# Kernel optimization log

Hardware: AMD Instinct MI355X
Metric: run time of the kernel (lower is better)

## Reference

```python
import jax, jax.numpy as jnp
import numpy as np

BATCH, LENGTH, IN, STATE, OUT = 8, 4096, 512, 256, 512


def setup_inputs() -> dict:
    key = jax.random.key(0)
    k1, k2, k3, k4, k5 = jax.random.split(key, 5)
    u = jax.random.normal(k1, (BATCH, LENGTH, IN), dtype=jnp.float32)
    x0 = jax.random.normal(k2, (BATCH, STATE), dtype=jnp.float32)
    A = 0.9999 * (2.0 * jax.random.uniform(k3, (STATE,), dtype=jnp.float32) - 1.0)
    B = jax.random.normal(k4, (IN, STATE), dtype=jnp.float32) / (STATE + IN) ** 0.5
    C = jax.random.normal(k5, (STATE, OUT), dtype=jnp.float32) / STATE ** 0.5
    return {"u": u, "x0": x0, "A": A, "B": B, "C": C}


def reference(u, x0, A, B, C):
    L = u.shape[1]
    # A_powers[t, n] = A[n] ** t, shape [L, state]
    A_powers = jnp.power(A[None, :], jnp.arange(L, dtype=u.dtype)[:, None])
    uB = u @ B  # [batch, L, state]
    # FFT convolution; inputs are real so rfft/irfft gives same result as
    # real(ifft(fft*fft)) in the original.
    T = 2 ** int(np.ceil(np.log2(2 * L - 1)))
    Af = jnp.fft.rfft(A_powers, n=T, axis=0)  # [T/2+1, state]
    Uf = jnp.fft.rfft(uB, n=T, axis=1)        # [batch, T/2+1, state]
    x = jnp.fft.irfft(Af[None, :, :] * Uf, n=T, axis=1)[:, :L]  # [batch, L, state]
    # initial-state contribution: A * A_powers * x0
    x = x + A[None, None, :] * A_powers[None, :, :] * x0[:, None, :]
    y = x @ C  # [batch, L, out]
    return (y, x[:, -1])
```

## Files before the change

kernel.cpp:

```cpp
#include <hip/hip_runtime.h>

#define BATCH   8
#define LENGTH  4096
#define IN_DIM  512
#define STATE   256
#define OUT_DIM 512
#define NC      64
#define LC      64

typedef __attribute__((ext_vector_type(8)))  short bf16x8;
typedef __attribute__((ext_vector_type(16))) float f32x16;

union FragU { bf16x8 v; unsigned u[4]; };

__device__ __forceinline__ unsigned short bf16_rne(float v) {
    unsigned u = __builtin_bit_cast(unsigned, v);
    unsigned r = (u + 0x7FFFu + ((u >> 16) & 1u)) >> 16;
    return (unsigned short)r;
}
__device__ __forceinline__ float bf16_f(unsigned short h) {
    unsigned u = ((unsigned)h) << 16;
    return __builtin_bit_cast(float, u);
}

__global__ __launch_bounds__(256) void split_T_kernel(
    const float* __restrict__ in, unsigned short* __restrict__ hi,
    unsigned short* __restrict__ lo, int kbits, int Nsrc)
{
    int id = blockIdx.x * 256 + threadIdx.x;
    int k = id & ((1 << kbits) - 1);
    int n = id >> kbits;
    float v = in[(size_t)k * Nsrc + n];
    unsigned short h = bf16_rne(v);
    hi[id] = h;
    lo[id] = bf16_rne(v - bf16_f(h));
}

__global__ __launch_bounds__(256, 2) void gemm_dbuf(
    const float* __restrict__ Af, const unsigned short* __restrict__ Bthi,
    const unsigned short* __restrict__ Btlo, float* __restrict__ Cc,
    int N_, int K)
{
    __shared__ unsigned short lds[2 * 16384];

    const int tid  = threadIdx.x;
    const int wave = tid >> 6;
    const int lane = tid & 63;
    const int n0 = blockIdx.x * 128;
    const int m0 = blockIdx.y * 128;

    const char* gp[8];
    int ldsoff[8], gstep[8];
    #pragma unroll
    for (int t = 0; t < 8; ++t) {
        int gi = wave * 8 + t;
        if (gi < 16) {
            int p = gi * 64 + lane;
            int row = p >> 3, s = p & 7;
            int l = s ^ (row & 7);
            gp[t] = (const char*)(Af + (size_t)(m0 + row) * K + l * 4);
            gstep[t] = 32 * 4;
            ldsoff[t] = gi * 512;
        } else {
            int q2 = (gi - 16) >> 3;
            int pi = (gi - 16) & 7;
            int p = pi * 64 + lane;
            int row = p >> 2, s = p & 3;
            int l = s ^ ((row >> 1) & 3);
            const unsigned short* base = q2 ? Btlo : Bthi;
            gp[t] = (const char*)(base + (size_t)(n0 + row) * K + l * 8);
            gstep[t] = 32 * 2;
            ldsoff[t] = 8192 + q2 * 4096 + pi * 512;
        }
    }

    const int l31 = lane & 31, q2 = lane >> 5;
    const int wm = (wave >> 1) * 64, wn = (wave & 1) * 64;

    int aoff[2][2][2];
    #pragma unroll
    for (int mi = 0; mi < 2; ++mi) {
        int row = wm + mi * 32 + l31;
        #pragma unroll
        for (int ks = 0; ks < 2; ++ks)
            #pragma unroll
            for (int h = 0; h < 2; ++h)
                aoff[mi][ks][h] = row * 64 + ((ks * 4 + q2 * 2 + h) ^ (row & 7)) * 8;
    }
    int boff[2][2];
    #pragma unroll
    for (int nj = 0; nj < 2; ++nj) {
        int row = wn + nj * 32 + l31;
        #pragma unroll
        for (int ks = 0; ks < 2; ++ks)
            boff[nj][ks] = row * 32 + (((ks * 2 + q2) ^ ((row >> 1) & 3))) * 8;
    }

    f32x16 acc[2][2];
    #pragma unroll
    for (int mi = 0; mi < 2; ++mi)
        #pragma unroll
        for (int nj = 0; nj < 2; ++nj)
            #pragma unroll
            for (int r = 0; r < 16; ++r) acc[mi][nj][r] = 0.f;

    #pragma unroll
    for (int t = 0; t < 8; ++t) {
        __builtin_amdgcn_global_load_lds(
            (const __attribute__((address_space(1))) unsigned*)(gp[t]),
            (__attribute__((address_space(3))) unsigned*)(&lds[ldsoff[t]]),
            16, 0, 0);
        gp[t] += gstep[t];
    }

    const int nit = K >> 5;
    for (int it = 0; it < nit; ++it) {
        asm volatile("" ::: "memory");
        __builtin_amdgcn_s_barrier();
        asm volatile("" ::: "memory");
        if (it + 1 < nit) {
            const int bb = ((it + 1) & 1) * 16384;
            #pragma unroll
            for (int t = 0; t < 8; ++t) {
                __builtin_amdgcn_global_load_lds(
                    (const __attribute__((address_space(1))) unsigned*)(gp[t]),
                    (__attribute__((address_space(3))) unsigned*)(&lds[bb + ldsoff[t]]),
                    16, 0, 0);
                gp[t] += gstep[t];
            }
            __builtin_amdgcn_s_waitcnt(0x0F78);
        } else {
            __builtin_amdgcn_s_waitcnt(0x0F70);
        }
        asm volatile("" ::: "memory");
        __builtin_amdgcn_s_barrier();
        asm volatile("" ::: "memory");

        const unsigned short* buf = &lds[(it & 1) * 16384];

        #pragma unroll
        for (int ks = 0; ks < 2; ++ks) {
            FragU ahi[2], alo[2];
            #pragma unroll
            for (int mi = 0; mi < 2; ++mi) {
                float4 f0 = *(const float4*)(buf + aoff[mi][ks][0]);
                float4 f1 = *(const float4*)(buf + aoff[mi][ks][1]);
                unsigned b0 = __builtin_bit_cast(unsigned, f0.x);
                unsigned b1 = __builtin_bit_cast(unsigned, f0.y);
                unsigned b2 = __builtin_bit_cast(unsigned, f0.z);
                unsigned b3 = __builtin_bit_cast(unsigned, f0.w);
                unsigned b4 = __builtin_bit_cast(unsigned, f1.x);
                unsigned b5 = __builtin_bit_cast(unsigned, f1.y);
                unsigned b6 = __builtin_bit_cast(unsigned, f1.z);
                unsigned b7 = __builtin_bit_cast(unsigned, f1.w);
                ahi[mi].u[0] = __builtin_amdgcn_perm(b1, b0, 0x07060302);
                ahi[mi].u[1] = __builtin_amdgcn_perm(b3, b2, 0x07060302);
                ahi[mi].u[2] = __builtin_amdgcn_perm(b5, b4, 0x07060302);
                ahi[mi].u[3] = __builtin_amdgcn_perm(b7, b6, 0x07060302);
                float l0 = f0.x - __builtin_bit_cast(float, b0 & 0xFFFF0000u);
                float l1 = f0.y - __builtin_bit_cast(float, b1 & 0xFFFF0000u);
                float l2 = f0.z - __builtin_bit_cast(float, b2 & 0xFFFF0000u);
                float l3 = f0.w - __builtin_bit_cast(float, b3 & 0xFFFF0000u);
                float l4 = f1.x - __builtin_bit_cast(float, b4 & 0xFFFF0000u);
                float l5 = f1.y - __builtin_bit_cast(float, b5 & 0xFFFF0000u);
                float l6 = f1.z - __builtin_bit_cast(float, b6 & 0xFFFF0000u);
                float l7 = f1.w - __builtin_bit_cast(float, b7 & 0xFFFF0000u);
                alo[mi].u[0] = __builtin_amdgcn_perm(
                    __builtin_bit_cast(unsigned, l1), __builtin_bit_cast(unsigned, l0), 0x07060302);
                alo[mi].u[1] = __builtin_amdgcn_perm(
                    __builtin_bit_cast(unsigned, l3), __builtin_bit_cast(unsigned, l2), 0x07060302);
                alo[mi].u[2] = __builtin_amdgcn_perm(
                    __builtin_bit_cast(unsigned, l5), __builtin_bit_cast(unsigned, l4), 0x07060302);
                alo[mi].u[3] = __builtin_amdgcn_perm(
                    __builtin_bit_cast(unsigned, l7), __builtin_bit_cast(unsigned, l6), 0x07060302);
            }
            FragU bhi[2], blo[2];
            #pragma unroll
            for (int nj = 0; nj < 2; ++nj) {
                bhi[nj].v = *(const bf16x8*)(buf +  8192 + boff[nj][ks]);
                blo[nj].v = *(const bf16x8*)(buf + 12288 + boff[nj][ks]);
            }
            #pragma unroll
            for (int mi = 0; mi < 2; ++mi)
                #pragma unroll
                for (int nj = 0; nj < 2; ++nj) {
                    acc[mi][nj] = __builtin_amdgcn_mfma_f32_32x32x16_bf16(
                        ahi[mi].v, bhi[nj].v, acc[mi][nj], 0, 0, 0);
                    acc[mi][nj] = __builtin_amdgcn_mfma_f32_32x32x16_bf16(
                        alo[mi].v, bhi[nj].v, acc[mi][nj], 0, 0, 0);
                    acc[mi][nj] = __builtin_amdgcn_mfma_f32_32x32x16_bf16(
                        ahi[mi].v, blo[nj].v, acc[mi][nj], 0, 0, 0);
                }
        }
    }

    #pragma unroll
    for (int mi = 0; mi < 2; ++mi)
        #pragma unroll
        for (int nj = 0; nj < 2; ++nj) {
            #pragma unroll
            for (int r = 0; r < 16; ++r) {
                int row_g = m0 + wm + mi * 32 + 4 * q2 + (r & 3) + 8 * (r >> 2);
                int col_g = n0 + wn + nj * 32 + l31;
                Cc[(size_t)row_g * N_ + col_g] = acc[mi][nj][r];
            }
        }
}

__global__ __launch_bounds__(256) void scan_carry(
    const float* __restrict__ uB, const float* __restrict__ A,
    float* __restrict__ carry)
{
    const int b = blockIdx.x;
    const int c = blockIdx.y;
    const int n = threadIdx.x;
    const float a = A[n];
    const float* p = uB + ((size_t)b * LENGTH + (size_t)c * LC) * STATE + n;
    float s = 0.f;
    #pragma unroll 8
    for (int j = 0; j < LC; ++j) s = a * s + p[(size_t)j * STATE];
    carry[((size_t)b * NC + c) * STATE + n] = s;
}

__global__ __launch_bounds__(256) void scan_apply(
    const float* __restrict__ uB, const float* __restrict__ A,
    const float* __restrict__ carry, const float* __restrict__ x0,
    float* __restrict__ x, float* __restrict__ x_last)
{
    const int b = blockIdx.x;
    const int c = blockIdx.y;
    const int n = threadIdx.x;
    const float a = A[n];
    float a2 = a * a, a4 = a2 * a2, a8 = a4 * a4, a16 = a8 * a8, a32 = a16 * a16;
    const float aLC = a32 * a32;

    float s = x0[(size_t)b * STATE + n];
    for (int d = 0; d < c; ++d)
        s = aLC * s + carry[((size_t)b * NC + d) * STATE + n];

    const size_t base = ((size_t)b * LENGTH + (size_t)c * LC) * STATE + n;
    const float* p = uB + base;
    float* qx = x + base;
    #pragma unroll 8
    for (int j = 0; j < LC; ++j) {
        s = a * s + p[(size_t)j * STATE];
        qx[(size_t)j * STATE] = s;
    }
    if (c == NC - 1) x_last[(size_t)b * STATE + n] = s;
}

extern "C" void kernel_launch(void* const* d_in, const int* in_sizes, int n_in,
                              void* d_out, int out_size, void* d_ws, size_t ws_size,
                              hipStream_t stream)
{
    const float* u  = (const float*)d_in[0];
    const float* x0 = (const float*)d_in[1];
    const float* A  = (const float*)d_in[2];
    const float* B  = (const float*)d_in[3];
    const float* C  = (const float*)d_in[4];

    const size_t MB = 1024 * 1024;
    char* ws = (char*)d_ws;

    float* x     = (float*)(ws);
    float* carry = (float*)(ws + 32 * MB);
    unsigned short* Bt_hi = (unsigned short*)(ws + 33 * MB);
    unsigned short* Bt_lo = (unsigned short*)(ws + 33 * MB + 256 * 1024);
    unsigned short* Ct_hi = (unsigned short*)(ws + 33 * MB + 512 * 1024);
    unsigned short* Ct_lo = (unsigned short*)(ws + 33 * MB + 768 * 1024);

    float* y      = (float*)d_out;
    float* x_last = y + (size_t)BATCH * LENGTH * OUT_DIM;
    float* uB     = (float*)((char*)d_out + 32 * MB);

    const int M = BATCH * LENGTH;

    split_T_kernel<<<dim3((IN_DIM * STATE) / 256), dim3(256), 0, stream>>>(B, Bt_hi, Bt_lo, 9, STATE);
    split_T_kernel<<<dim3((STATE * OUT_DIM) / 256), dim3(256), 0, stream>>>(C, Ct_hi, Ct_lo, 8, OUT_DIM);

    gemm_dbuf<<<dim3(STATE / 128, M / 128), dim3(256), 0, stream>>>(
        u, Bt_hi, Bt_lo, uB, STATE, IN_DIM);

    scan_carry<<<dim3(BATCH, NC), dim3(256), 0, stream>>>(uB, A, carry);
    scan_apply<<<dim3(BATCH, NC), dim3(256), 0, stream>>>(uB, A, carry, x0, x, x_last);

    gemm_dbuf<<<dim3(OUT_DIM / 128, M / 128), dim3(256), 0, stream>>>(
        x, Ct_hi, Ct_lo, y, OUT_DIM, STATE);
}
```

Before: 217.0 us.

## Stage GEMM tiles through registers and precompute scan chunk prefixes

The GEMM drops the double-buffered direct global-to-LDS loads. It now uses a single LDS buffer fed from register-staged float4 prefetches, so the next tile's global load overlaps compute on the current tile, and K becomes a template parameter. The scan adds a small per-batch combine kernel that computes each chunk's starting state once. This replaces the per-block serial loop over all earlier chunk carries inside scan_apply. The register staging costs extra VGPRs and adds more barriers per iteration, and the scan adds one more launch.

```diff
diff --git a/kernel.cpp b/kernel.cpp
--- a/kernel.cpp
+++ b/kernel.cpp
@@ -36,12 +36,12 @@
     lo[id] = bf16_rne(v - bf16_f(h));
 }
 
-__global__ __launch_bounds__(256, 2) void gemm_dbuf(
+template<int K>
+__global__ __launch_bounds__(256, 2) void gemm_stage(
     const float* __restrict__ Af, const unsigned short* __restrict__ Bthi,
-    const unsigned short* __restrict__ Btlo, float* __restrict__ Cc,
-    int N_, int K)
-{
-    __shared__ unsigned short lds[2 * 16384];
+    const unsigned short* __restrict__ Btlo, float* __restrict__ Cc, int N_)
+{
+    __shared__ unsigned short lds[16384];
 
     const int tid  = threadIdx.x;
     const int wave = tid >> 6;
@@ -50,27 +50,24 @@
     const int m0 = blockIdx.y * 128;
 
     const char* gp[8];
-    int ldsoff[8], gstep[8];
-    #pragma unroll
-    for (int t = 0; t < 8; ++t) {
-        int gi = wave * 8 + t;
-        if (gi < 16) {
-            int p = gi * 64 + lane;
-            int row = p >> 3, s = p & 7;
-            int l = s ^ (row & 7);
-            gp[t] = (const char*)(Af + (size_t)(m0 + row) * K + l * 4);
-            gstep[t] = 32 * 4;
-            ldsoff[t] = gi * 512;
+    int ldsb[8], gstep[8];
+    #pragma unroll
+    for (int i = 0; i < 8; ++i) {
+        int c = i * 256 + tid;
+        if (c < 1024) {
+            int row = c >> 3, sub = c & 7;
+            gp[i] = (const char*)(Af + (size_t)(m0 + row) * K) + sub * 16;
+            gstep[i] = 32 * 4;
+            ldsb[i] = row * 128 + ((sub ^ (row & 7)) * 16);
         } else {
-            int q2 = (gi - 16) >> 3;
-            int pi = (gi - 16) & 7;
-            int p = pi * 64 + lane;
-            int row = p >> 2, s = p & 3;
-            int l = s ^ ((row >> 1) & 3);
-            const unsigned short* base = q2 ? Btlo : Bthi;
-            gp[t] = (const char*)(base + (size_t)(n0 + row) * K + l * 8);
-            gstep[t] = 32 * 2;
-            ldsoff[t] = 8192 + q2 * 4096 + pi * 512;
+            int d = c - 1024;
+            int pl = d >> 9;
+            int e = d & 511;
+            int row = e >> 2, sub = e & 3;
+            const unsigned short* bsrc = pl ? Btlo : Bthi;
+            gp[i] = (const char*)(bsrc + (size_t)(n0 + row) * K) + sub * 16;
+            gstep[i] = 32 * 2;
+            ldsb[i] = 16384 + pl * 8192 + row * 64 + ((sub ^ ((row >> 1) & 3)) * 16);
         }
     }
 
@@ -104,47 +101,26 @@
             #pragma unroll
             for (int r = 0; r < 16; ++r) acc[mi][nj][r] = 0.f;
 
-    #pragma unroll
-    for (int t = 0; t < 8; ++t) {
-        __builtin_amdgcn_global_load_lds(
-            (const __attribute__((address_space(1))) unsigned*)(gp[t]),
-            (__attribute__((address_space(3))) unsigned*)(&lds[ldsoff[t]]),
-            16, 0, 0);
-        gp[t] += gstep[t];
-    }
-
-    const int nit = K >> 5;
-    for (int it = 0; it < nit; ++it) {
-        asm volatile("" ::: "memory");
-        __builtin_amdgcn_s_barrier();
-        asm volatile("" ::: "memory");
-        if (it + 1 < nit) {
-            const int bb = ((it + 1) & 1) * 16384;
-            #pragma unroll
-            for (int t = 0; t < 8; ++t) {
-                __builtin_amdgcn_global_load_lds(
-                    (const __attribute__((address_space(1))) unsigned*)(gp[t]),
-                    (__attribute__((address_space(3))) unsigned*)(&lds[bb + ldsoff[t]]),
-                    16, 0, 0);
-                gp[t] += gstep[t];
-            }
-            __builtin_amdgcn_s_waitcnt(0x0F78);
-        } else {
-            __builtin_amdgcn_s_waitcnt(0x0F70);
-        }
-        asm volatile("" ::: "memory");
-        __builtin_amdgcn_s_barrier();
-        asm volatile("" ::: "memory");
-
-        const unsigned short* buf = &lds[(it & 1) * 16384];
-
+    auto load_tile = [&](float4* s) {
+        #pragma unroll
+        for (int i = 0; i < 8; ++i) {
+            s[i] = *(const float4*)(gp[i]);
+            gp[i] += gstep[i];
+        }
+    };
+    auto store_tile = [&](const float4* s) {
+        #pragma unroll
+        for (int i = 0; i < 8; ++i)
+            *(float4*)((char*)lds + ldsb[i]) = s[i];
+    };
+    auto compute = [&]() {
         #pragma unroll
         for (int ks = 0; ks < 2; ++ks) {
             FragU ahi[2], alo[2];
             #pragma unroll
             for (int mi = 0; mi < 2; ++mi) {
-                float4 f0 = *(const float4*)(buf + aoff[mi][ks][0]);
-                float4 f1 = *(const float4*)(buf + aoff[mi][ks][1]);
+                float4 f0 = *(const float4*)(lds + aoff[mi][ks][0]);
+                float4 f1 = *(const float4*)(lds + aoff[mi][ks][1]);
                 unsigned b0 = __builtin_bit_cast(unsigned, f0.x);
                 unsigned b1 = __builtin_bit_cast(unsigned, f0.y);
                 unsigned b2 = __builtin_bit_cast(unsigned, f0.z);
@@ -177,8 +153,8 @@
             FragU bhi[2], blo[2];
             #pragma unroll
             for (int nj = 0; nj < 2; ++nj) {
-                bhi[nj].v = *(const bf16x8*)(buf +  8192 + boff[nj][ks]);
-                blo[nj].v = *(const bf16x8*)(buf + 12288 + boff[nj][ks]);
+                bhi[nj].v = *(const bf16x8*)(lds +  8192 + boff[nj][ks]);
+                blo[nj].v = *(const bf16x8*)(lds + 12288 + boff[nj][ks]);
             }
             #pragma unroll
             for (int mi = 0; mi < 2; ++mi)
@@ -192,6 +168,23 @@
                         ahi[mi].v, blo[nj].v, acc[mi][nj], 0, 0, 0);
                 }
         }
+    };
+
+    float4 sA[8], sB[8];
+    load_tile(sA);
+    constexpr int nit = K / 32;
+    #pragma unroll 1
+    for (int p = 0; p < nit / 2; ++p) {
+        __syncthreads();
+        store_tile(sA);
+        __syncthreads();
+        load_tile(sB);
+        compute();
+        __syncthreads();
+        store_tile(sB);
+        __syncthreads();
+        if (p + 1 < nit / 2) load_tile(sA);
+        compute();
     }
 
     #pragma unroll
@@ -222,22 +215,32 @@
     carry[((size_t)b * NC + c) * STATE + n] = s;
 }
 
+__global__ __launch_bounds__(256) void scan_combine(
+    const float* __restrict__ carry, const float* __restrict__ A,
+    const float* __restrict__ x0, float* __restrict__ h)
+{
+    const int b = blockIdx.x;
+    const int n = threadIdx.x;
+    const float a = A[n];
+    float a2 = a * a, a4 = a2 * a2, a8 = a4 * a4, a16 = a8 * a8, a32 = a16 * a16;
+    const float aLC = a32 * a32;
+    float s = x0[(size_t)b * STATE + n];
+    for (int c = 0; c < NC; ++c) {
+        h[((size_t)b * NC + c) * STATE + n] = s;
+        s = aLC * s + carry[((size_t)b * NC + c) * STATE + n];
+    }
+}
+
 __global__ __launch_bounds__(256) void scan_apply(
     const float* __restrict__ uB, const float* __restrict__ A,
-    const float* __restrict__ carry, const float* __restrict__ x0,
-    float* __restrict__ x, float* __restrict__ x_last)
+    const float* __restrict__ h, float* __restrict__ x,
+    float* __restrict__ x_last)
 {
     const int b = blockIdx.x;
     const int c = blockIdx.y;
     const int n = threadIdx.x;
     const float a = A[n];
-    float a2 = a * a, a4 = a2 * a2, a8 = a4 * a4, a16 = a8 * a8, a32 = a16 * a16;
-    const float aLC = a32 * a32;
-
-    float s = x0[(size_t)b * STATE + n];
-    for (int d = 0; d < c; ++d)
-        s = aLC * s + carry[((size_t)b * NC + d) * STATE + n];
-
+    float s = h[((size_t)b * NC + c) * STATE + n];
     const size_t base = ((size_t)b * LENGTH + (size_t)c * LC) * STATE + n;
     const float* p = uB + base;
     float* qx = x + base;
@@ -264,6 +267,7 @@
 
     float* x     = (float*)(ws);
     float* carry = (float*)(ws + 32 * MB);
+    float* h     = (float*)(ws + 32 * MB + 512 * 1024);
     unsigned short* Bt_hi = (unsigned short*)(ws + 33 * MB);
     unsigned short* Bt_lo = (unsigned short*)(ws + 33 * MB + 256 * 1024);
     unsigned short* Ct_hi = (unsigned short*)(ws + 33 * MB + 512 * 1024);
@@ -278,12 +282,13 @@
     split_T_kernel<<<dim3((IN_DIM * STATE) / 256), dim3(256), 0, stream>>>(B, Bt_hi, Bt_lo, 9, STATE);
     split_T_kernel<<<dim3((STATE * OUT_DIM) / 256), dim3(256), 0, stream>>>(C, Ct_hi, Ct_lo, 8, OUT_DIM);
 
-    gemm_dbuf<<<dim3(STATE / 128, M / 128), dim3(256), 0, stream>>>(
-        u, Bt_hi, Bt_lo, uB, STATE, IN_DIM);
-
-    scan_carry<<<dim3(BATCH, NC), dim3(256), 0, stream>>>(uB, A, carry);
-    scan_apply<<<dim3(BATCH, NC), dim3(256), 0, stream>>>(uB, A, carry, x0, x, x_last);
-
-    gemm_dbuf<<<dim3(OUT_DIM / 128, M / 128), dim3(256), 0, stream>>>(
-        x, Ct_hi, Ct_lo, y, OUT_DIM, STATE);
-}
+    gemm_stage<IN_DIM><<<dim3(STATE / 128, M / 128), dim3(256), 0, stream>>>(
+        u, Bt_hi, Bt_lo, uB, STATE);
+
+    scan_carry  <<<dim3(BATCH, NC), dim3(256), 0, stream>>>(uB, A, carry);
+    scan_combine<<<dim3(BATCH),     dim3(256), 0, stream>>>(carry, A, x0, h);
+    scan_apply  <<<dim3(BATCH, NC), dim3(256), 0, stream>>>(uB, A, h, x, x_last);
+
+    gemm_stage<STATE><<<dim3(OUT_DIM / 128, M / 128), dim3(256), 0, stream>>>(
+        x, Ct_hi, Ct_lo, y, OUT_DIM);
+}
```

After: 359.8 us. 1.66x slower.
